# Kernel optimization log

Hardware: AMD Instinct MI355X
Metric: run time of the kernel (lower is better)

The kernel has to match this reference:

```python
import jax, jax.numpy as jnp
import numpy as np

LATENT_DIM = 256
BOOK_SIZE = 8192


def setup_inputs() -> dict:
    key = jax.random.key(0)
    k1, k2 = jax.random.split(key)
    z_e = jax.random.normal(k1, (16, LATENT_DIM, 32, 32), dtype=jnp.float32)
    codebook = jax.random.normal(k2, (BOOK_SIZE, LATENT_DIM), dtype=jnp.float32)
    return {"z_e": z_e, "codebook": codebook}


def reference(z_e, codebook):
    # NCHW -> NHWC -> (B*H*W, D)
    flat_z = jnp.transpose(z_e, (0, 2, 3, 1)).reshape(-1, LATENT_DIM)
    # squared euclidean distance via matmul: ||z||^2 + ||e||^2 - 2 z.e
    dist = (
        jnp.sum(flat_z ** 2, axis=1, keepdims=True)
        + jnp.sum(codebook ** 2, axis=1)
        - 2.0 * flat_z @ codebook.T
    )  # (N, book_size)
    indices = jnp.argmin(dist, axis=1)          # (N,)
    z_q = codebook[indices]                      # (N, D) gather
    return z_q, indices
```

## Files before the change

kernel.cpp:

```cpp
#include <hip/hip_runtime.h>
#include <stdint.h>

#define NROWS 16384
#define NCODES 8192
#define DIM 256
#define EPS_S 0.4f
#define SM 0.8f

typedef __attribute__((ext_vector_type(8))) short bf16x8;
typedef __attribute__((ext_vector_type(16))) float f32x16;
typedef unsigned int uint32;

__device__ __forceinline__ unsigned short f2bf(float f) {
  union { float f; unsigned int u; } v; v.f = f;
  unsigned int u = v.u;
  return (unsigned short)((u + 0x7FFFu + ((u >> 16) & 1u)) >> 16);
}

__device__ __forceinline__ unsigned long long packdi(float d, int idx) {
  unsigned int u = __float_as_uint(d);
  u = (u & 0x80000000u) ? ~u : (u | 0x80000000u);
  return ((unsigned long long)u << 32) | (unsigned int)idx;
}
__device__ __forceinline__ unsigned long long u64min(unsigned long long a,
                                                     unsigned long long b) {
  return a < b ? a : b;
}
__device__ __forceinline__ unsigned long long shflx64(unsigned long long v, int m) {
  int lo = __shfl_xor((int)(unsigned int)v, m);
  int hi = __shfl_xor((int)(v >> 32), m);
  return ((unsigned long long)(unsigned int)hi << 32) | (unsigned int)lo;
}
__device__ __forceinline__ uint32 umax(uint32 a, uint32 b) { return a > b ? a : b; }
__device__ __forceinline__ uint32 umin(uint32 a, uint32 b) { return a < b ? a : b; }

__device__ __forceinline__ void glds16(const ushort* g, ushort* l) {
  __builtin_amdgcn_global_load_lds(
      (const __attribute__((address_space(1))) unsigned int*)g,
      (__attribute__((address_space(3))) unsigned int*)l, 16, 0, 0);
}

__global__ __launch_bounds__(256) void prep(const float* __restrict__ z,
                                            const float* __restrict__ cb,
                                            float* __restrict__ flatz,
                                            ushort* __restrict__ zb,
                                            ushort* __restrict__ eb,
                                            float* __restrict__ enorm) {
  __shared__ float t[32][33];
  const int blk = blockIdx.x;
  if (blk < 4096) {
    const int tx = threadIdx.x & 31, ty = threadIdx.x >> 5;
    const int ht = blk & 31, ct = (blk >> 5) & 7, b = blk >> 8;
    const float* src = z + (size_t)b * 262144 + (size_t)(ct * 32) * 1024 + ht * 32;
#pragma unroll
    for (int i = 0; i < 4; ++i) {
      int c = ty + i * 8;
      t[c][tx] = src[c * 1024 + tx];
    }
    __syncthreads();
#pragma unroll
    for (int i = 0; i < 4; ++i) {
      int hw = ty + i * 8;
      int row = b * 1024 + ht * 32 + hw;
      float v = t[tx][hw];
      flatz[(size_t)row * 256 + ct * 32 + tx] = v;
      zb[(size_t)row * 256 + ct * 32 + tx] = f2bf(v);
    }
  } else {
    const int lane = threadIdx.x & 63, wave = threadIdx.x >> 6;
    const int code = (blk - 4096) * 4 + wave;
    float4 v = *(const float4*)(cb + (size_t)code * 256 + lane * 4);
    ushort4 o;
    o.x = f2bf(v.x); o.y = f2bf(v.y); o.z = f2bf(v.z); o.w = f2bf(v.w);
    *(ushort4*)(eb + (size_t)code * 256 + lane * 4) = o;
    float ss = v.x * v.x + v.y * v.y + v.z * v.z + v.w * v.w;
#pragma unroll
    for (int s = 1; s < 64; s <<= 1) ss += __shfl_xor(ss, s);
    if (lane == 0) enorm[code] = ss;
  }
}

__global__ __launch_bounds__(512, 2) void vq_gemm(const ushort* __restrict__ eb,
                                                  const ushort* __restrict__ zb,
                                                  const float* __restrict__ enorm,
                                                  uint32* __restrict__ bm) {
  __shared__ __align__(16) ushort As[2][16384];
  __shared__ __align__(16) ushort Bs[2][16384];
  const int wave = threadIdx.x >> 6, lane = threadIdx.x & 63;
  const int wm = wave >> 2, wn = wave & 3;
  const int l31 = lane & 31, lg = lane >> 5;
  const int code0 = blockIdx.x * 256;
  const int zrow0 = blockIdx.y * 256;

  const int srow = wave * 8 + (lane >> 3);
  const int sslot = (lane & 7) ^ ((lane >> 3) & 7);
  const ushort* aSrc = eb + (size_t)(code0 + srow) * 256 + sslot * 8;
  const ushort* bSrc = zb + (size_t)(zrow0 + srow) * 256 + sslot * 8;
  const int ldst = wave * 512;

#pragma unroll
  for (int r = 0; r < 4; ++r) {
    glds16(aSrc + r * 16384, &As[0][r * 4096 + ldst]);
    glds16(bSrc + r * 16384, &Bs[0][r * 4096 + ldst]);
  }

  f32x16 acc[4][2];
#pragma unroll
  for (int m = 0; m < 4; ++m) {
    const float* ep = enorm + code0 + wm * 128 + m * 32 + 4 * lg;
    float4 e0 = *(const float4*)(ep);
    float4 e1 = *(const float4*)(ep + 8);
    float4 e2 = *(const float4*)(ep + 16);
    float4 e3 = *(const float4*)(ep + 24);
    f32x16 c0;
    c0[0]  = 1024.f - 0.5f * e0.x; c0[1]  = 1024.f - 0.5f * e0.y;
    c0[2]  = 1024.f - 0.5f * e0.z; c0[3]  = 1024.f - 0.5f * e0.w;
    c0[4]  = 1024.f - 0.5f * e1.x; c0[5]  = 1024.f - 0.5f * e1.y;
    c0[6]  = 1024.f - 0.5f * e1.z; c0[7]  = 1024.f - 0.5f * e1.w;
    c0[8]  = 1024.f - 0.5f * e2.x; c0[9]  = 1024.f - 0.5f * e2.y;
    c0[10] = 1024.f - 0.5f * e2.z; c0[11] = 1024.f - 0.5f * e2.w;
    c0[12] = 1024.f - 0.5f * e3.x; c0[13] = 1024.f - 0.5f * e3.y;
    c0[14] = 1024.f - 0.5f * e3.z; c0[15] = 1024.f - 0.5f * e3.w;
    acc[m][0] = c0; acc[m][1] = c0;
  }

  __syncthreads();

  int col[4];
#pragma unroll
  for (int ks = 0; ks < 4; ++ks)
    col[ks] = ((((ks << 1) | lg) ^ (lane & 7)) << 3);
  const int arow = (wm * 128 + l31) * 64;
  const int brow = (wn * 64 + l31) * 64;

  bf16x8 ab[2][4];
  bf16x8 bb0[4], bb1[4];

#pragma unroll
  for (int t = 0; t < 4; ++t) {
    const int cur = t & 1;
    const ushort* A = As[cur];
    const ushort* B = Bs[cur];
    ushort* An = As[cur ^ 1];
    ushort* Bn = Bs[cur ^ 1];
    const int ko = (t + 1) * 64;

#pragma unroll
    for (int mi = 0; mi < 2; ++mi)
#pragma unroll
      for (int ks = 0; ks < 4; ++ks)
        ab[mi][ks] = *(const bf16x8*)(A + arow + mi * 2048 + col[ks]);
#pragma unroll
    for (int ks = 0; ks < 4; ++ks)
      bb0[ks] = *(const bf16x8*)(B + brow + col[ks]);
    if (t < 3) {
      glds16(aSrc + 0 * 16384 + ko, An + 0 * 4096 + ldst);
      glds16(aSrc + 1 * 16384 + ko, An + 1 * 4096 + ldst);
      glds16(bSrc + 0 * 16384 + ko, Bn + 0 * 4096 + ldst);
      glds16(bSrc + 1 * 16384 + ko, Bn + 1 * 4096 + ldst);
    }
    __builtin_amdgcn_s_barrier();
    __builtin_amdgcn_s_setprio(1);
#pragma unroll
    for (int ks = 0; ks < 4; ++ks) {
      acc[0][0] = __builtin_amdgcn_mfma_f32_32x32x16_bf16(ab[0][ks], bb0[ks],
                                                          acc[0][0], 0, 0, 0);
      acc[1][0] = __builtin_amdgcn_mfma_f32_32x32x16_bf16(ab[1][ks], bb0[ks],
                                                          acc[1][0], 0, 0, 0);
    }
    __builtin_amdgcn_s_setprio(0);
    __builtin_amdgcn_s_barrier();

#pragma unroll
    for (int ks = 0; ks < 4; ++ks)
      bb1[ks] = *(const bf16x8*)(B + brow + 2048 + col[ks]);
    if (t < 3) {
      glds16(aSrc + 2 * 16384 + ko, An + 2 * 4096 + ldst);
      glds16(aSrc + 3 * 16384 + ko, An + 3 * 4096 + ldst);
      glds16(bSrc + 2 * 16384 + ko, Bn + 2 * 4096 + ldst);
      glds16(bSrc + 3 * 16384 + ko, Bn + 3 * 4096 + ldst);
    }
    __builtin_amdgcn_s_barrier();
    __builtin_amdgcn_s_setprio(1);
#pragma unroll
    for (int ks = 0; ks < 4; ++ks) {
      acc[0][1] = __builtin_amdgcn_mfma_f32_32x32x16_bf16(ab[0][ks], bb1[ks],
                                                          acc[0][1], 0, 0, 0);
      acc[1][1] = __builtin_amdgcn_mfma_f32_32x32x16_bf16(ab[1][ks], bb1[ks],
                                                          acc[1][1], 0, 0, 0);
    }
    __builtin_amdgcn_s_setprio(0);
    __builtin_amdgcn_s_barrier();

#pragma unroll
    for (int mi = 0; mi < 2; ++mi)
#pragma unroll
      for (int ks = 0; ks < 4; ++ks)
        ab[mi][ks] = *(const bf16x8*)(A + arow + (2 + mi) * 2048 + col[ks]);
    __builtin_amdgcn_s_barrier();
    __builtin_amdgcn_s_setprio(1);
#pragma unroll
    for (int ks = 0; ks < 4; ++ks) {
      acc[2][1] = __builtin_amdgcn_mfma_f32_32x32x16_bf16(ab[0][ks], bb1[ks],
                                                          acc[2][1], 0, 0, 0);
      acc[3][1] = __builtin_amdgcn_mfma_f32_32x32x16_bf16(ab[1][ks], bb1[ks],
                                                          acc[3][1], 0, 0, 0);
    }
    __builtin_amdgcn_s_setprio(0);
    __builtin_amdgcn_s_barrier();

    __builtin_amdgcn_s_setprio(1);
#pragma unroll
    for (int ks = 0; ks < 4; ++ks) {
      acc[2][0] = __builtin_amdgcn_mfma_f32_32x32x16_bf16(ab[0][ks], bb0[ks],
                                                          acc[2][0], 0, 0, 0);
      acc[3][0] = __builtin_amdgcn_mfma_f32_32x32x16_bf16(ab[1][ks], bb0[ks],
                                                          acc[3][0], 0, 0, 0);
    }
    __builtin_amdgcn_s_setprio(0);
    if (t < 3) __syncthreads();
  }

  const int cid0 = blockIdx.x * 16 + wm * 8;
#pragma unroll
  for (int n = 0; n < 2; ++n) {
    uint32 res[8];
#pragma unroll
    for (int m = 0; m < 4; ++m)
#pragma unroll
      for (int hc = 0; hc < 2; ++hc) {
        uint32 m1 = 0, m2 = 0;
#pragma unroll
        for (int p = 0; p < 8; ++p) {
          uint32 id = (uint32)((p & 3) | (lg << 2) | ((p >> 2) << 3));
          uint32 pv = (__float_as_uint(acc[m][n][hc * 8 + p]) & ~31u) | id;
          m2 = umax(m2, umin(m1, pv));
          m1 = umax(m1, pv);
        }
        uint32 o1 = (uint32)__shfl_xor((int)m1, 32);
        uint32 o2 = (uint32)__shfl_xor((int)m2, 32);
        m2 = umax(umax(m2, o2), umin(m1, o1));
        m1 = umax(m1, o1);
        float s1 = __uint_as_float(m1 & ~31u);
        float s2 = __uint_as_float(m2 & ~31u);
        res[m * 2 + hc] = (s1 - s2 > SM) ? (m1 | 16u) : m1;
      }
    const int zr = zrow0 + wn * 64 + n * 32 + l31;
    uint4 o;
    o.x = lg ? res[4] : res[0];
    o.y = lg ? res[5] : res[1];
    o.z = lg ? res[6] : res[2];
    o.w = lg ? res[7] : res[3];
    *(uint4*)(bm + (size_t)zr * 512 + cid0 + lg * 4) = o;
  }
}

__device__ __forceinline__ unsigned long long chunk_exact(
    int chunk, const float* __restrict__ zrow, const float* __restrict__ cb,
    const float* __restrict__ enorm, int lane) {
  const int code = chunk * 16 + (lane >> 2);
  const float* zp = zrow + (lane & 3) * 64;
  const float* cp = cb + (size_t)code * 256 + (lane & 3) * 64;
  float s = 0.f;
#pragma unroll
  for (int d = 0; d < 64; d += 4) {
    float4 zv = *(const float4*)(zp + d);
    float4 cv = *(const float4*)(cp + d);
    s = fmaf(zv.x, cv.x, s); s = fmaf(zv.y, cv.y, s);
    s = fmaf(zv.z, cv.z, s); s = fmaf(zv.w, cv.w, s);
  }
  s += __shfl_xor(s, 1);
  s += __shfl_xor(s, 2);
  float dist = fmaf(-2.f, s, enorm[code]);
  unsigned long long key = ((lane & 3) == 0) ? packdi(dist, code) : ~0ull;
#pragma unroll
  for (int m = 1; m < 64; m <<= 1) key = u64min(key, shflx64(key, m));
  return key;
}

__global__ __launch_bounds__(256) void vq_sel(const uint32* __restrict__ bm,
                                              const float* __restrict__ flatz,
                                              const float* __restrict__ cb,
                                              const float* __restrict__ enorm,
                                              float* __restrict__ zq,
                                              float* __restrict__ oidx) {
  const int lane = threadIdx.x & 63;
  const int row = blockIdx.x * 4 + (threadIdx.x >> 6);
  uint4 va = *(const uint4*)(bm + (size_t)row * 512 + lane * 8);
  uint4 vb = *(const uint4*)(bm + (size_t)row * 512 + lane * 8 + 4);
  uint32 v[8] = {va.x, va.y, va.z, va.w, vb.x, vb.y, vb.z, vb.w};
  uint32 m1 = 0, m2 = 0; int ch = 0;
#pragma unroll
  for (int s = 0; s < 8; ++s) {
    uint32 pv = v[s];
    m2 = umax(m2, umin(m1, pv));
    ch = (pv > m1) ? (lane * 8 + s) : ch;
    m1 = umax(m1, pv);
  }
#pragma unroll
  for (int m = 1; m < 64; m <<= 1) {
    uint32 o1 = (uint32)__shfl_xor((int)m1, m);
    uint32 o2 = (uint32)__shfl_xor((int)m2, m);
    int oc = __shfl_xor(ch, m);
    m2 = umax(umax(m2, o2), umin(m1, o1));
    ch = (o1 > m1) ? oc : ch;
    m1 = umax(m1, o1);
  }
  float s1 = __uint_as_float(m1 & ~31u);
  float s2 = __uint_as_float(m2 & ~31u);
  int idx;
  if ((m1 & 16u) && (s1 - s2 > SM)) {
    idx = ch * 16 + (int)(m1 & 15u);
  } else {
    const float* zrow = flatz + (size_t)row * 256;
    unsigned long long key = chunk_exact(ch, zrow, cb, enorm, lane);
    float dbest;
    { unsigned int u = (unsigned int)(key >> 32);
      u = (u & 0x80000000u) ? (u & 0x7FFFFFFFu) : ~u;
      dbest = __uint_as_float(u); }
    float thr = (1024.f - 0.5f * dbest) - EPS_S;
#pragma unroll
    for (int s = 0; s < 8; ++s) {
      bool cand = __uint_as_float(v[s] & ~31u) >= thr;
      unsigned long long mk = __ballot(cand);
      while (mk) {
        int L = __ffsll(mk) - 1;
        mk &= mk - 1;
        int c2 = L * 8 + s;
        if (c2 == ch) continue;
        key = u64min(key, chunk_exact(c2, zrow, cb, enorm, lane));
      }
    }
    idx = (int)(key & 0xFFFFFFFFull);
  }
  if (lane == 0) oidx[row] = (float)idx;
  float4 val = *(const float4*)(cb + (size_t)idx * 256 + lane * 4);
  *(float4*)(zq + (size_t)row * 256 + lane * 4) = val;
}

extern "C" void kernel_launch(void* const* d_in, const int* in_sizes, int n_in,
                              void* d_out, int out_size, void* d_ws, size_t ws_size,
                              hipStream_t stream) {
  const float* z = (const float*)d_in[0];
  const float* cb = (const float*)d_in[1];
  char* ws = (char*)d_ws;
  ushort* zb = (ushort*)(ws);
  ushort* eb = (ushort*)(ws + (8u << 20));
  float* enorm = (float*)(ws + (12u << 20));
  uint32* bm = (uint32*)(ws + (13u << 20));
  float* zq = (float*)d_out;
  float* oidx = zq + (size_t)NROWS * DIM;
  float* flatz = zq;

  prep<<<4096 + NCODES / 4, 256, 0, stream>>>(z, cb, flatz, zb, eb, enorm);
  vq_gemm<<<dim3(NCODES / 256, NROWS / 256), 512, 0, stream>>>(eb, zb, enorm, bm);
  vq_sel<<<NROWS / 4, 256, 0, stream>>>(bm, flatz, cb, enorm, zq, oidx);
}
```

Measured before the change: 199.7 us.

## Make vq_gemm persistent over code tiles with a four-stage async LDS pipeline

The GEMM now launches 256 blocks, and each block loops over 8 consecutive 256-code tiles for one 256-row z tile. Loads are split into 32-wide K chunks in a 4-slot ring, prefetched two chunks ahead with explicit vmcnt waits. This overlaps one tile's epilogue and the next tile's first loads, and removes the per-tile prologue and launch cost. The code norms are staged once in LDS. Risks are fewer blocks per CU, higher LDS use (about 136KB, which may limit occupancy) and hand-counted waitcnts that must stay exactly right.

Measured after the change: 197.9 us. No clear change (-0.9%).

```diff
diff --git a/kernel.cpp b/kernel.cpp
--- a/kernel.cpp
+++ b/kernel.cpp
@@ -80,34 +80,11 @@
   }
 }
 
-__global__ __launch_bounds__(512, 2) void vq_gemm(const ushort* __restrict__ eb,
-                                                  const ushort* __restrict__ zb,
-                                                  const float* __restrict__ enorm,
-                                                  uint32* __restrict__ bm) {
-  __shared__ __align__(16) ushort As[2][16384];
-  __shared__ __align__(16) ushort Bs[2][16384];
-  const int wave = threadIdx.x >> 6, lane = threadIdx.x & 63;
-  const int wm = wave >> 2, wn = wave & 3;
-  const int l31 = lane & 31, lg = lane >> 5;
-  const int code0 = blockIdx.x * 256;
-  const int zrow0 = blockIdx.y * 256;
-
-  const int srow = wave * 8 + (lane >> 3);
-  const int sslot = (lane & 7) ^ ((lane >> 3) & 7);
-  const ushort* aSrc = eb + (size_t)(code0 + srow) * 256 + sslot * 8;
-  const ushort* bSrc = zb + (size_t)(zrow0 + srow) * 256 + sslot * 8;
-  const int ldst = wave * 512;
-
-#pragma unroll
-  for (int r = 0; r < 4; ++r) {
-    glds16(aSrc + r * 16384, &As[0][r * 4096 + ldst]);
-    glds16(bSrc + r * 16384, &Bs[0][r * 4096 + ldst]);
-  }
-
-  f32x16 acc[4][2];
+__device__ __forceinline__ void init_acc(f32x16 acc[4][2], const float* en,
+                                         int ot, int wm, int lg) {
 #pragma unroll
   for (int m = 0; m < 4; ++m) {
-    const float* ep = enorm + code0 + wm * 128 + m * 32 + 4 * lg;
+    const float* ep = en + ot * 256 + wm * 128 + m * 32 + 4 * lg;
     float4 e0 = *(const float4*)(ep);
     float4 e1 = *(const float4*)(ep + 8);
     float4 e2 = *(const float4*)(ep + 16);
@@ -123,105 +100,13 @@
     c0[14] = 1024.f - 0.5f * e3.z; c0[15] = 1024.f - 0.5f * e3.w;
     acc[m][0] = c0; acc[m][1] = c0;
   }
-
-  __syncthreads();
-
-  int col[4];
-#pragma unroll
-  for (int ks = 0; ks < 4; ++ks)
-    col[ks] = ((((ks << 1) | lg) ^ (lane & 7)) << 3);
-  const int arow = (wm * 128 + l31) * 64;
-  const int brow = (wn * 64 + l31) * 64;
-
-  bf16x8 ab[2][4];
-  bf16x8 bb0[4], bb1[4];
-
-#pragma unroll
-  for (int t = 0; t < 4; ++t) {
-    const int cur = t & 1;
-    const ushort* A = As[cur];
-    const ushort* B = Bs[cur];
-    ushort* An = As[cur ^ 1];
-    ushort* Bn = Bs[cur ^ 1];
-    const int ko = (t + 1) * 64;
-
-#pragma unroll
-    for (int mi = 0; mi < 2; ++mi)
-#pragma unroll
-      for (int ks = 0; ks < 4; ++ks)
-        ab[mi][ks] = *(const bf16x8*)(A + arow + mi * 2048 + col[ks]);
-#pragma unroll
-    for (int ks = 0; ks < 4; ++ks)
-      bb0[ks] = *(const bf16x8*)(B + brow + col[ks]);
-    if (t < 3) {
-      glds16(aSrc + 0 * 16384 + ko, An + 0 * 4096 + ldst);
-      glds16(aSrc + 1 * 16384 + ko, An + 1 * 4096 + ldst);
-      glds16(bSrc + 0 * 16384 + ko, Bn + 0 * 4096 + ldst);
-      glds16(bSrc + 1 * 16384 + ko, Bn + 1 * 4096 + ldst);
-    }
-    __builtin_amdgcn_s_barrier();
-    __builtin_amdgcn_s_setprio(1);
-#pragma unroll
-    for (int ks = 0; ks < 4; ++ks) {
-      acc[0][0] = __builtin_amdgcn_mfma_f32_32x32x16_bf16(ab[0][ks], bb0[ks],
-                                                          acc[0][0], 0, 0, 0);
-      acc[1][0] = __builtin_amdgcn_mfma_f32_32x32x16_bf16(ab[1][ks], bb0[ks],
-                                                          acc[1][0], 0, 0, 0);
-    }
-    __builtin_amdgcn_s_setprio(0);
-    __builtin_amdgcn_s_barrier();
-
-#pragma unroll
-    for (int ks = 0; ks < 4; ++ks)
-      bb1[ks] = *(const bf16x8*)(B + brow + 2048 + col[ks]);
-    if (t < 3) {
-      glds16(aSrc + 2 * 16384 + ko, An + 2 * 4096 + ldst);
-      glds16(aSrc + 3 * 16384 + ko, An + 3 * 4096 + ldst);
-      glds16(bSrc + 2 * 16384 + ko, Bn + 2 * 4096 + ldst);
-      glds16(bSrc + 3 * 16384 + ko, Bn + 3 * 4096 + ldst);
-    }
-    __builtin_amdgcn_s_barrier();
-    __builtin_amdgcn_s_setprio(1);
-#pragma unroll
-    for (int ks = 0; ks < 4; ++ks) {
-      acc[0][1] = __builtin_amdgcn_mfma_f32_32x32x16_bf16(ab[0][ks], bb1[ks],
-                                                          acc[0][1], 0, 0, 0);
-      acc[1][1] = __builtin_amdgcn_mfma_f32_32x32x16_bf16(ab[1][ks], bb1[ks],
-                                                          acc[1][1], 0, 0, 0);
-    }
-    __builtin_amdgcn_s_setprio(0);
-    __builtin_amdgcn_s_barrier();
-
-#pragma unroll
-    for (int mi = 0; mi < 2; ++mi)
-#pragma unroll
-      for (int ks = 0; ks < 4; ++ks)
-        ab[mi][ks] = *(const bf16x8*)(A + arow + (2 + mi) * 2048 + col[ks]);
-    __builtin_amdgcn_s_barrier();
-    __builtin_amdgcn_s_setprio(1);
-#pragma unroll
-    for (int ks = 0; ks < 4; ++ks) {
-      acc[2][1] = __builtin_amdgcn_mfma_f32_32x32x16_bf16(ab[0][ks], bb1[ks],
-                                                          acc[2][1], 0, 0, 0);
-      acc[3][1] = __builtin_amdgcn_mfma_f32_32x32x16_bf16(ab[1][ks], bb1[ks],
-                                                          acc[3][1], 0, 0, 0);
-    }
-    __builtin_amdgcn_s_setprio(0);
-    __builtin_amdgcn_s_barrier();
-
-    __builtin_amdgcn_s_setprio(1);
-#pragma unroll
-    for (int ks = 0; ks < 4; ++ks) {
-      acc[2][0] = __builtin_amdgcn_mfma_f32_32x32x16_bf16(ab[0][ks], bb0[ks],
-                                                          acc[2][0], 0, 0, 0);
-      acc[3][0] = __builtin_amdgcn_mfma_f32_32x32x16_bf16(ab[1][ks], bb0[ks],
-                                                          acc[3][0], 0, 0, 0);
-    }
-    __builtin_amdgcn_s_setprio(0);
-    if (t < 3) __syncthreads();
-  }
-
-  const int cid0 = blockIdx.x * 16 + wm * 8;
+}
+
+__device__ __forceinline__ void epilogue(const f32x16 acc[4][2],
+                                         uint32* __restrict__ bm, int cg,
+                                         int ot, int zrow0, int wm, int wn,
+                                         int l31, int lg) {
+  const int cid0 = cg * 128 + ot * 16 + wm * 8;
 #pragma unroll
   for (int n = 0; n < 2; ++n) {
     uint32 res[8];
@@ -255,6 +140,122 @@
   }
 }
 
+__global__ __launch_bounds__(512, 2) void vq_gemm(const ushort* __restrict__ eb,
+                                                  const ushort* __restrict__ zb,
+                                                  const float* __restrict__ enorm,
+                                                  uint32* __restrict__ bm) {
+  __shared__ __align__(16) ushort As[4 * 8192];
+  __shared__ __align__(16) ushort Bs[4 * 8192];
+  __shared__ __align__(16) float en[2048];
+  const int tid = threadIdx.x;
+  const int wave = tid >> 6, lane = tid & 63;
+  const int wm = wave >> 2, wn = wave & 3;
+  const int l31 = lane & 31, lg = lane >> 5;
+  const int y = blockIdx.x & 63, cg = blockIdx.x >> 6;
+  const int code00 = cg * 2048;
+  const int zrow0 = y * 256;
+
+  *(float4*)&en[tid * 4] = *(const float4*)(enorm + code00 + tid * 4);
+  __syncthreads();
+
+  const int u0 = tid, u1 = tid + 512;
+  const ushort* aU0 = eb + (size_t)(code00 + (u0 >> 2)) * 256 +
+                      ((u0 & 3) ^ ((u0 >> 2) & 3)) * 8;
+  const ushort* aU1 = eb + (size_t)(code00 + (u1 >> 2)) * 256 +
+                      ((u1 & 3) ^ ((u1 >> 2) & 3)) * 8;
+  const ushort* bU0 = zb + (size_t)(zrow0 + (u0 >> 2)) * 256 +
+                      ((u0 & 3) ^ ((u0 >> 2) & 3)) * 8;
+  const ushort* bU1 = zb + (size_t)(zrow0 + (u1 >> 2)) * 256 +
+                      ((u1 & 3) ^ ((u1 >> 2) & 3)) * 8;
+  ushort* aL = As + wave * 512;
+  ushort* bL = Bs + wave * 512;
+
+  glds16(aU0, aL);
+  glds16(aU1, aL + 4096);
+  glds16(bU0, bL);
+  glds16(bU1, bL + 4096);
+  glds16(aU0 + 32, aL + 8192);
+  glds16(aU1 + 32, aL + 8192 + 4096);
+  glds16(bU0 + 32, bL + 8192);
+  glds16(bU1 + 32, bL + 8192 + 4096);
+
+  f32x16 acc[4][2];
+  init_acc(acc, en, 0, wm, lg);
+
+  asm volatile("s_waitcnt vmcnt(4)" ::: "memory");
+  __builtin_amdgcn_s_barrier();
+  asm volatile("" ::: "memory");
+
+  const int sw = lane & 3;
+  const int colu0 = ((0 | lg) ^ sw) * 8;
+  const int colu1 = ((2 | lg) ^ sw) * 8;
+  const int arow_u = (wm * 128 + l31) * 32;
+  const int brow_u = (wn * 64 + l31) * 32;
+
+#pragma unroll 1
+  for (int ot = 0; ot < 8; ++ot) {
+    const size_t aoff = (size_t)ot * 65536;
+    if (ot > 0) {
+      epilogue(acc, bm, cg, ot - 1, zrow0, wm, wn, l31, lg);
+      init_acc(acc, en, ot, wm, lg);
+    }
+#pragma unroll
+    for (int cc = 0; cc < 8; ++cc) {
+      const int slot = cc & 3;
+      if (cc < 6) {
+        const int s2 = (cc + 2) & 3;
+        const int ko = (cc + 2) * 32;
+        glds16(aU0 + aoff + ko, aL + s2 * 8192);
+        glds16(aU1 + aoff + ko, aL + s2 * 8192 + 4096);
+        glds16(bU0 + ko, bL + s2 * 8192);
+        glds16(bU1 + ko, bL + s2 * 8192 + 4096);
+      } else if (ot < 7) {
+        const int s2 = (cc + 2) & 3;
+        const int ko = (cc - 6) * 32;
+        glds16(aU0 + aoff + 65536 + ko, aL + s2 * 8192);
+        glds16(aU1 + aoff + 65536 + ko, aL + s2 * 8192 + 4096);
+        glds16(bU0 + ko, bL + s2 * 8192);
+        glds16(bU1 + ko, bL + s2 * 8192 + 4096);
+      }
+      bf16x8 a0[4], a1[4], b0[2], b1[2];
+#pragma unroll
+      for (int m = 0; m < 4; ++m) {
+        a0[m] = *(const bf16x8*)&As[slot * 8192 + arow_u + m * 1024 + colu0];
+        a1[m] = *(const bf16x8*)&As[slot * 8192 + arow_u + m * 1024 + colu1];
+      }
+#pragma unroll
+      for (int n = 0; n < 2; ++n) {
+        b0[n] = *(const bf16x8*)&Bs[slot * 8192 + brow_u + n * 1024 + colu0];
+        b1[n] = *(const bf16x8*)&Bs[slot * 8192 + brow_u + n * 1024 + colu1];
+      }
+      __builtin_amdgcn_s_setprio(1);
+#pragma unroll
+      for (int m = 0; m < 4; ++m)
+#pragma unroll
+        for (int n = 0; n < 2; ++n)
+          acc[m][n] = __builtin_amdgcn_mfma_f32_32x32x16_bf16(a0[m], b0[n],
+                                                              acc[m][n], 0, 0, 0);
+#pragma unroll
+      for (int m = 0; m < 4; ++m)
+#pragma unroll
+        for (int n = 0; n < 2; ++n)
+          acc[m][n] = __builtin_amdgcn_mfma_f32_32x32x16_bf16(a1[m], b1[n],
+                                                              acc[m][n], 0, 0, 0);
+      __builtin_amdgcn_s_setprio(0);
+      if (cc < 6) {
+        asm volatile("s_waitcnt vmcnt(4)" ::: "memory");
+      } else if (ot < 7) {
+        asm volatile("s_waitcnt vmcnt(4)" ::: "memory");
+      } else {
+        asm volatile("s_waitcnt vmcnt(0)" ::: "memory");
+      }
+      __builtin_amdgcn_s_barrier();
+      asm volatile("" ::: "memory");
+    }
+  }
+  epilogue(acc, bm, cg, 7, zrow0, wm, wn, l31, lg);
+}
+
 __device__ __forceinline__ unsigned long long chunk_exact(
     int chunk, const float* __restrict__ zrow, const float* __restrict__ cb,
     const float* __restrict__ enorm, int lane) {
@@ -353,6 +354,6 @@
   float* flatz = zq;
 
   prep<<<4096 + NCODES / 4, 256, 0, stream>>>(z, cb, flatz, zb, eb, enorm);
-  vq_gemm<<<dim3(NCODES / 256, NROWS / 256), 512, 0, stream>>>(eb, zb, enorm, bm);
+  vq_gemm<<<256, 512, 0, stream>>>(eb, zb, enorm, bm);
   vq_sel<<<NROWS / 4, 256, 0, stream>>>(bm, flatz, cb, enorm, zq, oidx);
 }
```
